# Kernel tuning notes

Hardware: AMD Instinct MI355X
Metric: run time of the kernel (lower is better)

The kernel has to match this reference:

```python
import jax, jax.numpy as jnp
import numpy as np

COMMITMENT_COST = 0.25
CODEBOOK_SIZE = 8192
D_MODEL = 512


def setup_inputs() -> dict:
    key = jax.random.key(0)
    k1, k2 = jax.random.split(key)
    z = jax.random.normal(k1, (32, 1024, D_MODEL), dtype=jnp.float32)
    # embedding initialized uniform(-1/codebook_size, 1/codebook_size) like the torch module
    emb = jax.random.uniform(k2, (CODEBOOK_SIZE, D_MODEL), dtype=jnp.float32,
                             minval=-1.0 / CODEBOOK_SIZE, maxval=1.0 / CODEBOOK_SIZE)
    return {"z": z, "emb": emb}


def reference(z, emb):
    B, P, D = z.shape
    flat = z.reshape(-1, D)  # [N, D], N = B*P
    distances = (jnp.sum(flat * flat, axis=1, keepdims=True)
                 + jnp.sum(emb * emb, axis=1)
                 - 2.0 * jnp.matmul(flat, emb.T))
    indices = jnp.argmin(distances, axis=1)  # [N]
    quantized = emb[indices]  # [N, D] codebook gather
    e_latent_loss = jnp.mean((jax.lax.stop_gradient(quantized) - flat) ** 2)
    q_latent_loss = jnp.mean((quantized - jax.lax.stop_gradient(flat)) ** 2)
    loss = q_latent_loss + COMMITMENT_COST * e_latent_loss
    # straight-through estimator
    quantized_st = flat + jax.lax.stop_gradient(quantized - flat)
    return (loss, quantized_st.reshape(B, P, D), indices.reshape(B, P))
```

## Files before the change

kernel.cpp:

```cpp
#include <hip/hip_runtime.h>
#include <stdint.h>

#define NROWS 32768
#define DDIM  512
#define KCODES 8192
#define CAP 128
#define MARGIN_SCALED 5000
#define SZ 16.0f
#define SE 1040384.0f

#define OFF_ZQ   0
#define OFF_EQ   16777216
#define OFF_RMAX 20971520
#define OFF_CCNT 21102592
#define OFF_CIDX 21233664
#define OFF_LOSS 38010880

typedef __attribute__((ext_vector_type(4))) float floatx4;
typedef __attribute__((ext_vector_type(4))) int   intx4;

__device__ __forceinline__ unsigned fmap(float f) {
    unsigned u = __float_as_uint(f);
    return (u & 0x80000000u) ? ~u : (u | 0x80000000u);
}
__device__ __forceinline__ signed char q8(float v, float s) {
    int x = __float2int_rn(v * s);
    x = x > 127 ? 127 : (x < -127 ? -127 : x);
    return (signed char)x;
}

__global__ __launch_bounds__(256) void k_setup(const float* __restrict__ z,
                                               const float* __restrict__ emb,
                                               signed char* __restrict__ zq,
                                               signed char* __restrict__ eq,
                                               int* __restrict__ rmax,
                                               unsigned* __restrict__ ccnt,
                                               double* __restrict__ loss) {
    const int bid = blockIdx.x, t = threadIdx.x;
    {
        const int i = (bid * 256 + t) * 8;
        floatx4 a = *(const floatx4*)(z + i);
        floatx4 b = *(const floatx4*)(z + i + 4);
        unsigned long long p = 0;
#pragma unroll
        for (int j = 0; j < 4; j++) {
            p |= (unsigned long long)(unsigned char)q8(a[j], SZ) << (8 * j);
            p |= (unsigned long long)(unsigned char)q8(b[j], SZ) << (8 * (j + 4));
        }
        *(unsigned long long*)(zq + i) = p;
    }
    if (bid < 2048) {
        const int i = (bid * 256 + t) * 8;
        floatx4 a = *(const floatx4*)(emb + i);
        floatx4 b = *(const floatx4*)(emb + i + 4);
        unsigned long long p = 0;
#pragma unroll
        for (int j = 0; j < 4; j++) {
            p |= (unsigned long long)(unsigned char)q8(a[j], SE) << (8 * j);
            p |= (unsigned long long)(unsigned char)q8(b[j], SE) << (8 * (j + 4));
        }
        *(unsigned long long*)(eq + i) = p;
    }
    if (bid < 64) {
        const int i = bid * 256 + t;
        rmax[i] = (int)0x80000000; rmax[i + 16384] = (int)0x80000000;
        ccnt[i] = 0u;              ccnt[i + 16384] = 0u;
    }
    if (bid == 0 && t == 0) *loss = 0.0;
}

__global__ __launch_bounds__(512, 2) void k_gemm(const signed char* __restrict__ zq,
                                                 const signed char* __restrict__ eq,
                                                 int* __restrict__ rowmaxI,
                                                 unsigned* __restrict__ candCnt,
                                                 unsigned* __restrict__ candIdx) {
    __shared__ signed char lds[131072];
    __shared__ int sMaxI[256];
    __shared__ int sThrI[256];

    const int t = threadIdx.x;
    const int w = t >> 6;
    const int l = t & 63;
    const int wr = w >> 1, wc = w & 1;
    const int lr = l & 15, lg = l >> 4;

    const int bid = blockIdx.x;
    const int xcd = bid & 7, n = bid >> 3;
    const int rowT  = (xcd * 16 + (n & 15)) * 256;
    const int codeT = (n >> 4) * 256;

    const int sr   = t >> 3;
    const int sc16 = t & 7;
    const int scsw = (sc16 ^ (sr & 7)) * 16;

    intx4 acc0[4][4], acc1[4][4];
#pragma unroll
    for (int m = 0; m < 4; m++)
#pragma unroll
        for (int nn = 0; nn < 4; nn++) {
            acc0[m][nn] = (intx4){0, 0, 0, 0};
            acc1[m][nn] = (intx4){0, 0, 0, 0};
        }

    intx4 afr[4][2];
    intx4 bfr[4][2];

#define STAGE(kt, unit, bsel)                                                          \
    do {                                                                               \
        const signed char* _g = ((unit) < 4)                                           \
            ? zq + (size_t)(rowT  + (unit) * 64 + sr) * DDIM + (kt) * 128 + scsw       \
            : eq + (size_t)(codeT + ((unit) - 4) * 64 + sr) * DDIM + (kt) * 128 + scsw;\
        signed char* _d = ((unit) < 4)                                                 \
            ? lds + (bsel) * 32768 + ((unit) * 64 + sr) * 128 + sc16 * 16              \
            : lds + 65536 + (bsel) * 32768 + (((unit) - 4) * 64 + sr) * 128 + sc16 * 16;\
        __builtin_amdgcn_global_load_lds(                                              \
            (const __attribute__((address_space(1))) unsigned int*)_g,                 \
            (__attribute__((address_space(3))) unsigned int*)_d, 16, 0, 0);            \
    } while (0)

#define LDA(bsel)                                                                      \
    do {                                                                               \
        const signed char* _A = lds + (bsel) * 32768;                                  \
        _Pragma("unroll")                                                              \
        for (int _m = 0; _m < 4; _m++) {                                               \
            const int _row = wr * 64 + _m * 16 + lr;                                   \
            _Pragma("unroll")                                                          \
            for (int _ks = 0; _ks < 2; _ks++)                                          \
                afr[_m][_ks] = *(const intx4*)(_A + _row * 128 +                       \
                                (((_ks * 4 + lg) ^ (lr & 7)) * 16));                   \
        }                                                                              \
    } while (0)

#define LDB(bsel, h)                                                                   \
    do {                                                                               \
        const signed char* _B = lds + 65536 + (bsel) * 32768;                          \
        _Pragma("unroll")                                                              \
        for (int _nn = 0; _nn < 4; _nn++) {                                            \
            const int _row = wc * 128 + (h) * 64 + _nn * 16 + lr;                      \
            _Pragma("unroll")                                                          \
            for (int _ks = 0; _ks < 2; _ks++)                                          \
                bfr[_nn][_ks] = *(const intx4*)(_B + _row * 128 +                      \
                                (((_ks * 4 + lg) ^ (lr & 7)) * 16));                   \
        }                                                                              \
    } while (0)

#define MFMAH(accH)                                                                    \
    do {                                                                               \
        __builtin_amdgcn_s_setprio(1);                                                 \
        _Pragma("unroll")                                                              \
        for (int _m = 0; _m < 4; _m++)                                                 \
            _Pragma("unroll")                                                          \
            for (int _ks = 0; _ks < 2; _ks++)                                          \
                _Pragma("unroll")                                                      \
                for (int _nn = 0; _nn < 4; _nn++)                                      \
                    accH[_m][_nn] = __builtin_amdgcn_mfma_i32_16x16x64_i8(             \
                        afr[_m][_ks], bfr[_nn][_ks], accH[_m][_nn], 0, 0, 0);          \
        __builtin_amdgcn_s_setprio(0);                                                 \
    } while (0)

#define BAR() __builtin_amdgcn_s_barrier()
#define LGKM0() do { asm volatile("s_waitcnt lgkmcnt(0)" ::: "memory"); \
                     __builtin_amdgcn_sched_barrier(0); } while (0)
#define VMC8() do { asm volatile("s_waitcnt vmcnt(8)" ::: "memory"); \
                    __builtin_amdgcn_sched_barrier(0); } while (0)
#define CLMP(x) ((x) < 3 ? (x) : 3)

    if (t < 256) sMaxI[t] = (int)0x80000000;

    STAGE(0, 0, 0); STAGE(0, 1, 0); STAGE(0, 2, 0); STAGE(0, 3, 0);
    STAGE(0, 4, 0); STAGE(0, 5, 0); STAGE(0, 6, 0); STAGE(0, 7, 0);
    STAGE(1, 0, 1); STAGE(1, 1, 1); STAGE(1, 2, 1); STAGE(1, 3, 1);
    STAGE(1, 4, 1); STAGE(1, 5, 1); STAGE(1, 6, 1); STAGE(1, 7, 1);
    VMC8();
    BAR();

#pragma unroll 2
    for (int t0 = 0; t0 < 4; ++t0) {
        const int b  = t0 & 1;
        const int nk = CLMP(t0 + 2);
        LDA(b);
        LDB(b, 0);
        LGKM0();
        BAR();
        STAGE(nk, 0, b); STAGE(nk, 1, b); STAGE(nk, 2, b); STAGE(nk, 3, b);
        STAGE(nk, 4, b); STAGE(nk, 6, b);
        MFMAH(acc0);
        LDB(b, 1);
        LGKM0();
        BAR();
        STAGE(nk, 5, b); STAGE(nk, 7, b);
        MFMAH(acc1);
        VMC8();
        BAR();
    }

    __syncthreads();

#pragma unroll
    for (int m = 0; m < 4; m++) {
#pragma unroll
        for (int j = 0; j < 4; j++) {
            int v = max(max(max(acc0[m][0][j], acc0[m][1][j]),
                            max(acc0[m][2][j], acc0[m][3][j])),
                        max(max(acc1[m][0][j], acc1[m][1][j]),
                            max(acc1[m][2][j], acc1[m][3][j])));
#pragma unroll
            for (int s = 1; s < 16; s <<= 1) v = max(v, __shfl_xor(v, s, 64));
            if (lr == 0)
                atomicMax(&sMaxI[wr * 64 + m * 16 + lg * 4 + j], v);
        }
    }
    __syncthreads();
    if (t < 256) {
        int g  = rowmaxI[rowT + t];
        int tm = sMaxI[t];
        sThrI[t] = (tm > g ? tm : g) - MARGIN_SCALED;
        atomicMax(&rowmaxI[rowT + t], tm);
    }
    __syncthreads();

#pragma unroll
    for (int m = 0; m < 4; m++) {
#pragma unroll
        for (int j = 0; j < 4; j++) {
            const int rl = wr * 64 + m * 16 + lg * 4 + j;
            const int thr = sThrI[rl];
#pragma unroll
            for (int h = 0; h < 2; h++) {
#pragma unroll
                for (int nn = 0; nn < 4; nn++) {
                    int d = h ? acc1[m][nn][j] : acc0[m][nn][j];
                    if (d >= thr) {
                        unsigned pos = atomicAdd(&candCnt[rowT + rl], 1u);
                        if (pos < CAP)
                            candIdx[(size_t)(rowT + rl) * CAP + pos] =
                                (unsigned)(codeT + wc * 128 + h * 64 + nn * 16 + lr);
                    }
                }
            }
        }
    }
#undef STAGE
#undef LDA
#undef LDB
#undef MFMAH
#undef BAR
#undef LGKM0
#undef VMC8
#undef CLMP
}

__global__ __launch_bounds__(256) void k_rescore(const float* __restrict__ z,
                                                 const float* __restrict__ emb,
                                                 const unsigned* __restrict__ candCnt,
                                                 unsigned* __restrict__ candIdx,
                                                 float* __restrict__ out) {
    const int w = threadIdx.x >> 6, l = threadIdx.x & 63;
    const int row = blockIdx.x * 4 + w;
    const int g = l >> 3, q = l & 7;
    const float* zr = z + (size_t)row * DDIM;

    floatx4 za  = *(const floatx4*)(zr + l * 8);
    floatx4 zb4 = *(const floatx4*)(zr + l * 8 + 4);
    double s1 = 0.0;
#pragma unroll
    for (int j = 0; j < 4; j++) { s1 += (double)za[j] * za[j]; s1 += (double)zb4[j] * zb4[j]; }
#pragma unroll
    for (int s = 1; s < 64; s <<= 1) s1 += __shfl_xor(s1, s, 64);
    const float s1f = (float)s1;

    floatx4 zq[16];
#pragma unroll
    for (int k = 0; k < 16; k++) zq[k] = *(const floatx4*)(zr + q * 64 + k * 4);

    auto score = [&](unsigned c) -> unsigned long long {
        const float* er = emb + (size_t)c * DDIM + q * 64;
        double dt = 0.0;
#pragma unroll
        for (int k = 0; k < 16; k++) {
            floatx4 e = *(const floatx4*)(er + k * 4);
            dt += (double)zq[k][0] * (double)e[0];
            dt += (double)zq[k][1] * (double)e[1];
            dt += (double)zq[k][2] * (double)e[2];
            dt += (double)zq[k][3] * (double)e[3];
        }
        dt += __shfl_xor(dt, 1, 64);
        dt += __shfl_xor(dt, 2, 64);
        dt += __shfl_xor(dt, 4, 64);
        float uf = (float)(2.0 * dt);
        float df = s1f - uf;
        return ((unsigned long long)fmap(df) << 32) | (unsigned long long)c;
    };

    unsigned cnt = candCnt[row];
    unsigned long long best = ~0ull;
    if (cnt <= CAP) {
        for (unsigned i = g; i < cnt; i += 8) {
            unsigned long long k = score(candIdx[(size_t)row * CAP + i]);
            best = k < best ? k : best;
        }
    } else {
        for (unsigned c = g; c < KCODES; c += 8) {
            unsigned long long k = score(c);
            best = k < best ? k : best;
        }
    }
#pragma unroll
    for (int s = 8; s < 64; s <<= 1) {
        unsigned long long o = __shfl_xor(best, s, 64);
        best = o < best ? o : best;
    }
    const unsigned idx = (unsigned)best;

    const float* er = emb + (size_t)idx * DDIM + l * 8;
    float* oq = out + 1 + (size_t)row * DDIM + l * 8;
    double lp = 0.0;
#pragma unroll
    for (int j = 0; j < 8; j++) {
        float zv = (j < 4) ? za[j] : zb4[j - 4];
        float qv = er[j];
        oq[j] = zv + (qv - zv);
        double d = (double)qv - (double)zv;
        lp += d * d;
    }
#pragma unroll
    for (int s = 1; s < 64; s <<= 1) lp += __shfl_xor(lp, s, 64);
    if (l == 0) {
        out[1 + 16777216 + row] = (float)idx;
        ((double*)(candIdx + (size_t)row * CAP))[0] = lp;
    }
}

__global__ __launch_bounds__(256) void k_lossred(const unsigned* __restrict__ candIdx,
                                                 double* __restrict__ lossAcc) {
    const int tid = blockIdx.x * 256 + threadIdx.x;
    double s = ((const double*)(candIdx + (size_t)tid * CAP))[0]
             + ((const double*)(candIdx + (size_t)(tid + 16384) * CAP))[0];
#pragma unroll
    for (int sh = 1; sh < 64; sh <<= 1) s += __shfl_xor(s, sh, 64);
    __shared__ double partial[4];
    const int l = threadIdx.x & 63, w = threadIdx.x >> 6;
    if (l == 0) partial[w] = s;
    __syncthreads();
    if (threadIdx.x == 0)
        atomicAdd(lossAcc, partial[0] + partial[1] + partial[2] + partial[3]);
}

__global__ void k_final(const double* __restrict__ lossAcc, float* __restrict__ out) {
    if (threadIdx.x == 0 && blockIdx.x == 0)
        out[0] = (float)(1.25 * (*lossAcc) * (1.0 / 16777216.0));
}

extern "C" void kernel_launch(void* const* d_in, const int* in_sizes, int n_in,
                              void* d_out, int out_size, void* d_ws, size_t ws_size,
                              hipStream_t stream) {
    const float* z   = (const float*)d_in[0];
    const float* emb = (const float*)d_in[1];
    float* out = (float*)d_out;
    char* ws = (char*)d_ws;
    signed char* zq = (signed char*)(ws + OFF_ZQ);
    signed char* eq = (signed char*)(ws + OFF_EQ);
    int* rmax = (int*)(ws + OFF_RMAX);
    unsigned* ccnt = (unsigned*)(ws + OFF_CCNT);
    unsigned* cidx = (unsigned*)(ws + OFF_CIDX);
    double* loss = (double*)(ws + OFF_LOSS);

    k_setup<<<dim3(8192), 256, 0, stream>>>(z, emb, zq, eq, rmax, ccnt, loss);
    k_gemm<<<dim3(4096), 512, 0, stream>>>(zq, eq, rmax, ccnt, cidx);
    k_rescore<<<dim3(NROWS / 4), 256, 0, stream>>>(z, emb, ccnt, cidx, out);
    k_lossred<<<dim3(64), 256, 0, stream>>>(cidx, loss);
    k_final<<<dim3(1), 64, 0, stream>>>(loss, out);
}
```

Baseline: 465.4 us.

## Shrink int8 GEMM block tile from 256x256 to 128x128 with 4 waves

The int8 MFMA distance GEMM moves from 512-thread blocks computing a 256x256 row-by-code tile to 256-thread blocks computing 128x128 tiles, with four times as many blocks. LDS use is halved and per-thread accumulators drop from two 4x4 sets to one, and the fragment loads are merged into one phase per k-step with staging split around two MFMA halves. This should improve occupancy and shorten the tail, but it lowers arithmetic intensity and per-tile operand reuse. It also doubles the global rowmax atomics and loads across code tiles, which could make the GEMM more memory-bound.

```diff
diff --git a/kernel.cpp b/kernel.cpp
--- a/kernel.cpp
+++ b/kernel.cpp
@@ -69,14 +69,14 @@
     if (bid == 0 && t == 0) *loss = 0.0;
 }
 
-__global__ __launch_bounds__(512, 2) void k_gemm(const signed char* __restrict__ zq,
+__global__ __launch_bounds__(256, 2) void k_gemm(const signed char* __restrict__ zq,
                                                  const signed char* __restrict__ eq,
                                                  int* __restrict__ rowmaxI,
                                                  unsigned* __restrict__ candCnt,
                                                  unsigned* __restrict__ candIdx) {
-    __shared__ signed char lds[131072];
-    __shared__ int sMaxI[256];
-    __shared__ int sThrI[256];
+    __shared__ signed char lds[65536];
+    __shared__ int sMaxI[128];
+    __shared__ int sThrI[128];
 
     const int t = threadIdx.x;
     const int w = t >> 6;
@@ -86,21 +86,18 @@
 
     const int bid = blockIdx.x;
     const int xcd = bid & 7, n = bid >> 3;
-    const int rowT  = (xcd * 16 + (n & 15)) * 256;
-    const int codeT = (n >> 4) * 256;
+    const int rowT  = (xcd * 32 + (n & 31)) * 128;
+    const int codeT = (n >> 5) * 128;
 
     const int sr   = t >> 3;
     const int sc16 = t & 7;
     const int scsw = (sc16 ^ (sr & 7)) * 16;
 
-    intx4 acc0[4][4], acc1[4][4];
+    intx4 acc[4][4];
 #pragma unroll
     for (int m = 0; m < 4; m++)
 #pragma unroll
-        for (int nn = 0; nn < 4; nn++) {
-            acc0[m][nn] = (intx4){0, 0, 0, 0};
-            acc1[m][nn] = (intx4){0, 0, 0, 0};
-        }
+        for (int nn = 0; nn < 4; nn++) acc[m][nn] = (intx4){0, 0, 0, 0};
 
     intx4 afr[4][2];
     intx4 bfr[4][2];
@@ -108,19 +105,20 @@
 #define STAGE(kt, unit, bsel)                                                          \
     do {                                                                               \
         const signed char* _g = ((unit) < 4)                                           \
-            ? zq + (size_t)(rowT  + (unit) * 64 + sr) * DDIM + (kt) * 128 + scsw       \
-            : eq + (size_t)(codeT + ((unit) - 4) * 64 + sr) * DDIM + (kt) * 128 + scsw;\
+            ? zq + (size_t)(rowT  + (unit) * 32 + sr) * DDIM + (kt) * 128 + scsw       \
+            : eq + (size_t)(codeT + ((unit) - 4) * 32 + sr) * DDIM + (kt) * 128 + scsw;\
         signed char* _d = ((unit) < 4)                                                 \
-            ? lds + (bsel) * 32768 + ((unit) * 64 + sr) * 128 + sc16 * 16              \
-            : lds + 65536 + (bsel) * 32768 + (((unit) - 4) * 64 + sr) * 128 + sc16 * 16;\
+            ? lds + (bsel) * 16384 + ((unit) * 32 + sr) * 128 + sc16 * 16              \
+            : lds + 32768 + (bsel) * 16384 + (((unit) - 4) * 32 + sr) * 128 + sc16 * 16;\
         __builtin_amdgcn_global_load_lds(                                              \
             (const __attribute__((address_space(1))) unsigned int*)_g,                 \
             (__attribute__((address_space(3))) unsigned int*)_d, 16, 0, 0);            \
     } while (0)
 
-#define LDA(bsel)                                                                      \
+#define LOADFRAGS(bsel)                                                                \
     do {                                                                               \
-        const signed char* _A = lds + (bsel) * 32768;                                  \
+        const signed char* _A = lds + (bsel) * 16384;                                  \
+        const signed char* _B = lds + 32768 + (bsel) * 16384;                          \
         _Pragma("unroll")                                                              \
         for (int _m = 0; _m < 4; _m++) {                                               \
             const int _row = wr * 64 + _m * 16 + lr;                                   \
@@ -129,14 +127,9 @@
                 afr[_m][_ks] = *(const intx4*)(_A + _row * 128 +                       \
                                 (((_ks * 4 + lg) ^ (lr & 7)) * 16));                   \
         }                                                                              \
-    } while (0)
-
-#define LDB(bsel, h)                                                                   \
-    do {                                                                               \
-        const signed char* _B = lds + 65536 + (bsel) * 32768;                          \
         _Pragma("unroll")                                                              \
         for (int _nn = 0; _nn < 4; _nn++) {                                            \
-            const int _row = wc * 128 + (h) * 64 + _nn * 16 + lr;                      \
+            const int _row = wc * 64 + _nn * 16 + lr;                                  \
             _Pragma("unroll")                                                          \
             for (int _ks = 0; _ks < 2; _ks++)                                          \
                 bfr[_nn][_ks] = *(const intx4*)(_B + _row * 128 +                      \
@@ -144,17 +137,17 @@
         }                                                                              \
     } while (0)
 
-#define MFMAH(accH)                                                                    \
+#define MFMAH(m0)                                                                      \
     do {                                                                               \
         __builtin_amdgcn_s_setprio(1);                                                 \
         _Pragma("unroll")                                                              \
-        for (int _m = 0; _m < 4; _m++)                                                 \
+        for (int _mm = 0; _mm < 2; _mm++)                                              \
             _Pragma("unroll")                                                          \
             for (int _ks = 0; _ks < 2; _ks++)                                          \
                 _Pragma("unroll")                                                      \
                 for (int _nn = 0; _nn < 4; _nn++)                                      \
-                    accH[_m][_nn] = __builtin_amdgcn_mfma_i32_16x16x64_i8(             \
-                        afr[_m][_ks], bfr[_nn][_ks], accH[_m][_nn], 0, 0, 0);          \
+                    acc[(m0) + _mm][_nn] = __builtin_amdgcn_mfma_i32_16x16x64_i8(      \
+                        afr[(m0) + _mm][_ks], bfr[_nn][_ks], acc[(m0) + _mm][_nn], 0, 0, 0); \
         __builtin_amdgcn_s_setprio(0);                                                 \
     } while (0)
 
@@ -165,7 +158,7 @@
                     __builtin_amdgcn_sched_barrier(0); } while (0)
 #define CLMP(x) ((x) < 3 ? (x) : 3)
 
-    if (t < 256) sMaxI[t] = (int)0x80000000;
+    if (t < 128) sMaxI[t] = (int)0x80000000;
 
     STAGE(0, 0, 0); STAGE(0, 1, 0); STAGE(0, 2, 0); STAGE(0, 3, 0);
     STAGE(0, 4, 0); STAGE(0, 5, 0); STAGE(0, 6, 0); STAGE(0, 7, 0);
@@ -178,18 +171,13 @@
     for (int t0 = 0; t0 < 4; ++t0) {
         const int b  = t0 & 1;
         const int nk = CLMP(t0 + 2);
-        LDA(b);
-        LDB(b, 0);
+        LOADFRAGS(b);
         LGKM0();
         BAR();
         STAGE(nk, 0, b); STAGE(nk, 1, b); STAGE(nk, 2, b); STAGE(nk, 3, b);
-        STAGE(nk, 4, b); STAGE(nk, 6, b);
-        MFMAH(acc0);
-        LDB(b, 1);
-        LGKM0();
-        BAR();
-        STAGE(nk, 5, b); STAGE(nk, 7, b);
-        MFMAH(acc1);
+        MFMAH(0);
+        STAGE(nk, 4, b); STAGE(nk, 5, b); STAGE(nk, 6, b); STAGE(nk, 7, b);
+        MFMAH(2);
         VMC8();
         BAR();
     }
@@ -200,10 +188,8 @@
     for (int m = 0; m < 4; m++) {
 #pragma unroll
         for (int j = 0; j < 4; j++) {
-            int v = max(max(max(acc0[m][0][j], acc0[m][1][j]),
-                            max(acc0[m][2][j], acc0[m][3][j])),
-                        max(max(acc1[m][0][j], acc1[m][1][j]),
-                            max(acc1[m][2][j], acc1[m][3][j])));
+            int v = max(max(acc[m][0][j], acc[m][1][j]),
+                        max(acc[m][2][j], acc[m][3][j]));
 #pragma unroll
             for (int s = 1; s < 16; s <<= 1) v = max(v, __shfl_xor(v, s, 64));
             if (lr == 0)
@@ -211,7 +197,7 @@
         }
     }
     __syncthreads();
-    if (t < 256) {
+    if (t < 128) {
         int g  = rowmaxI[rowT + t];
         int tm = sMaxI[t];
         sThrI[t] = (tm > g ? tm : g) - MARGIN_SCALED;
@@ -226,23 +212,19 @@
             const int rl = wr * 64 + m * 16 + lg * 4 + j;
             const int thr = sThrI[rl];
 #pragma unroll
-            for (int h = 0; h < 2; h++) {
-#pragma unroll
-                for (int nn = 0; nn < 4; nn++) {
-                    int d = h ? acc1[m][nn][j] : acc0[m][nn][j];
-                    if (d >= thr) {
-                        unsigned pos = atomicAdd(&candCnt[rowT + rl], 1u);
-                        if (pos < CAP)
-                            candIdx[(size_t)(rowT + rl) * CAP + pos] =
-                                (unsigned)(codeT + wc * 128 + h * 64 + nn * 16 + lr);
-                    }
+            for (int nn = 0; nn < 4; nn++) {
+                int d = acc[m][nn][j];
+                if (d >= thr) {
+                    unsigned pos = atomicAdd(&candCnt[rowT + rl], 1u);
+                    if (pos < CAP)
+                        candIdx[(size_t)(rowT + rl) * CAP + pos] =
+                            (unsigned)(codeT + wc * 64 + nn * 16 + lr);
                 }
             }
         }
     }
 #undef STAGE
-#undef LDA
-#undef LDB
+#undef LOADFRAGS
 #undef MFMAH
 #undef BAR
 #undef LGKM0
@@ -366,7 +348,7 @@
     double* loss = (double*)(ws + OFF_LOSS);
 
     k_setup<<<dim3(8192), 256, 0, stream>>>(z, emb, zq, eq, rmax, ccnt, loss);
-    k_gemm<<<dim3(4096), 512, 0, stream>>>(zq, eq, rmax, ccnt, cidx);
+    k_gemm<<<dim3(16384), 256, 0, stream>>>(zq, eq, rmax, ccnt, cidx);
     k_rescore<<<dim3(NROWS / 4), 256, 0, stream>>>(z, emb, ccnt, cidx, out);
     k_lossred<<<dim3(64), 256, 0, stream>>>(cidx, loss);
     k_final<<<dim3(1), 64, 0, stream>>>(loss, out);
```

Result: slower. 515.3 us (+10.7%).
